# Performance work log

Hardware: AMD Instinct MI355X
Metric: run time of the kernel (lower is better)

## Reference

```python
import jax, jax.numpy as jnp
import numpy as np

GRID_SIZE = 5
SPLINE_ORDER = 3
GRID_LO, GRID_HI = -1.0, 1.0
N_COEFF = GRID_SIZE + SPLINE_ORDER  # 8


def make_grid(in_features):
    # (in_features, grid_size + 2*spline_order + 1) = (in, 12)
    h = (GRID_HI - GRID_LO) / GRID_SIZE
    g = jnp.arange(-SPLINE_ORDER, GRID_SIZE + SPLINE_ORDER + 1, dtype=jnp.float32) * h + GRID_LO
    return jnp.broadcast_to(g, (in_features, g.shape[0]))


def b_splines(x, grid):
    # x: (N, in); grid: (in, G). Returns (N, in, grid_size+spline_order).
    xe = x[..., None]
    bases = ((xe >= grid[:, :-1]) & (xe < grid[:, 1:])).astype(x.dtype)
    for k in range(1, SPLINE_ORDER + 1):
        left = (xe - grid[:, :-(k + 1)]) / (grid[:, k:-1] - grid[:, :-(k + 1)]) * bases[..., :-1]
        right = (grid[:, k + 1:] - xe) / (grid[:, k + 1:] - grid[:, 1:-k]) * bases[..., 1:]
        bases = left + right
    return bases


def kan_linear(x, base_w, spline_w, scaler, grid):
    # base branch: SiLU(x) @ base_w^T
    base_out = jax.nn.silu(x) @ base_w.T
    # spline branch: basis (N,in,c) contracted with scaled spline weight (out,in,c)
    b = b_splines(x, grid)
    sw = spline_w * scaler[..., None]
    spline_out = jnp.einsum('nic,oic->no', b, sw)
    return base_out + spline_out


def setup_inputs() -> dict:
    key = jax.random.key(0)
    ks = jax.random.split(key, 7)
    d_model, d_hid = 512, 2049  # d_ff + 1
    s = 0.1  # keep activations roughly inside grid range
    return {
        "x": jax.random.normal(ks[0], (4096, d_model), dtype=jnp.float32) * 0.3,
        "base_w1": jax.random.normal(ks[1], (d_hid, d_model), dtype=jnp.float32) * s,
        "spline_w1": jax.random.normal(ks[2], (d_hid, d_model, N_COEFF), dtype=jnp.float32) * s,
        "scaler1": jax.random.normal(ks[3], (d_hid, d_model), dtype=jnp.float32) * s,
        "base_w2": jax.random.normal(ks[4], (d_model, d_hid), dtype=jnp.float32) * s,
        "spline_w2": jax.random.normal(ks[5], (d_model, d_hid, N_COEFF), dtype=jnp.float32) * s,
        "scaler2": jax.random.normal(ks[6], (d_model, d_hid), dtype=jnp.float32) * s,
    }


def reference(x, base_w1, spline_w1, scaler1, base_w2, spline_w2, scaler2):
    grid1 = make_grid(x.shape[-1])
    h = kan_linear(x, base_w1, spline_w1, scaler1, grid1)
    grid2 = make_grid(h.shape[-1])
    out = kan_linear(h, base_w2, spline_w2, scaler2, grid2)
    return out
```

## Files before the change

kernel.cpp:

```cpp
#include <hip/hip_runtime.h>
#include <hip/hip_bf16.h>

#define T_TOK 4096
#define I1    512
#define O1    2049
#define O1P   2176
#define K1    4608
#define G1    64
#define I2    2049
#define O2    512
#define K2    18560
#define G2    271
#define SPLITS2 8
#define KLEN2 2368
#define NBY   32

typedef __attribute__((ext_vector_type(8))) short short8;
typedef __attribute__((ext_vector_type(4))) float floatx4;
typedef __attribute__((address_space(3))) void* lds_ptr_t;
typedef const __attribute__((address_space(1))) void* gmem_ptr_t;

__device__ __forceinline__ unsigned short f2bf(float f) {
  union { __hip_bfloat16 h; unsigned short u; } cv;
  cv.h = __float2bfloat16(f);
  return cv.u;
}
__device__ __forceinline__ unsigned bfr(float f) {
  union { float f; unsigned u; } c; c.f = f;
  return (c.u + 0x8000u) >> 16;
}
__device__ __forceinline__ float silu_f(float x) { return x / (1.0f + __expf(-x)); }

__device__ __forceinline__ uint4 spline_pack(float h) {
  float u = (h + 2.2f) * 2.5f;
  int ji = (int)u;
  ji = ji < 0 ? 0 : (ji > 10 ? 10 : ji);
  float t = u - (float)ji;
  float it = 1.0f - t, t2 = t * t, t3 = t2 * t;
  float b0 = it * it * it * (1.0f / 6.0f);
  float b1 = (3.0f * t3 - 6.0f * t2 + 4.0f) * (1.0f / 6.0f);
  float b2 = (-3.0f * t3 + 3.0f * t2 + 3.0f * t + 1.0f) * (1.0f / 6.0f);
  float b3 = t3 * (1.0f / 6.0f);
  unsigned pk01 = bfr(b0) | (bfr(b1) << 16);
  unsigned pk23 = bfr(b2) | (bfr(b3) << 16);
  unsigned long long p64 = (unsigned long long)pk01 | ((unsigned long long)pk23 << 32);
  bool inR = (h >= -2.2f) && (h < 2.2f);
  p64 = inR ? p64 : 0ull;
  int sh = (ji - 3) * 16;
  int shr = sh < 0 ? -sh : 0;
  int shl = sh < 0 ? 0 : sh;
  __uint128_t v = ((__uint128_t)(p64 >> shr)) << shl;
  union { __uint128_t q; uint4 u4; } cv;
  cv.q = v;
  return cv.u4;
}

__global__ void transpose_kernel(const float* __restrict__ src, float* __restrict__ dst,
                                 int R, int C) {
  __shared__ float t[32][33];
  int c0 = blockIdx.x * 32, r0 = blockIdx.y * 32;
  int tx = threadIdx.x & 31, ty = threadIdx.x >> 5;
#pragma unroll
  for (int i = 0; i < 32; i += 8)
    t[ty + i][tx] = src[(size_t)(r0 + ty + i) * C + c0 + tx];
  __syncthreads();
#pragma unroll
  for (int i = 0; i < 32; i += 8)
    dst[(size_t)(c0 + ty + i) * R + r0 + tx] = t[tx][ty + i];
}

__global__ void silu_pack_kernel(const float* __restrict__ St, uint4* __restrict__ SPK,
                                 int I, int M) {
  int m = blockIdx.x * 256 + threadIdx.x;
  int g = blockIdx.y;
  int off0 = g * 8;
  union { unsigned short s[8]; uint4 v; } pk;
#pragma unroll
  for (int c = 0; c < 8; ++c) {
    int off = off0 + c;
    float v = 0.0f;
    if (off < I) v = silu_f(St[(size_t)off * M + m]);
    pk.s[c] = f2bf(v);
  }
  SPK[(size_t)g * M + m] = pk.v;
}

__global__ void pack_w1_kernel(const float* __restrict__ bw, const float* __restrict__ sw,
                               const float* __restrict__ sc, unsigned short* __restrict__ W) {
  int k = blockIdx.x * 256 + threadIdx.x;
  int o = blockIdx.y;
  float v = 0.0f;
  if (o < O1) {
    if (k < 4096) v = sw[(size_t)o * 4096 + k] * sc[(size_t)o * I1 + (k >> 3)];
    else          v = bw[(size_t)o * I1 + (k - 4096)];
  }
  W[(size_t)o * K1 + k] = f2bf(v);
}

__global__ void pack_w2_kernel(const float* __restrict__ bw, const float* __restrict__ sw,
                               const float* __restrict__ sc, unsigned short* __restrict__ W) {
  int k = blockIdx.x * 256 + threadIdx.x;
  if (k >= K2) return;
  int o = blockIdx.y;
  float v = 0.0f;
  if (k < 16392)      v = sw[(size_t)o * 16392 + k] * sc[(size_t)o * I2 + (k >> 3)];
  else if (k < 18441) v = bw[(size_t)o * I2 + (k - 16392)];
  W[(size_t)o * K2 + k] = f2bf(v);
}

__global__ __launch_bounds__(256, 4)
void kan_gemm_kernel(const float* __restrict__ St, const uint4* __restrict__ SPK,
                     const unsigned short* __restrict__ Bw, float* __restrict__ C,
                     int I, int Ktot, int M, int N, int ldc, int kLen,
                     int nBx, int storeMode)
{
  __shared__ __align__(16) unsigned short As[128 * 64];
  __shared__ __align__(16) unsigned short Bs[128 * 64];

  const int Lb = blockIdx.x;
  const int m8 = Lb & 7;
  const int r  = Lb >> 3;
  const int bx = r % nBx;
  const int p  = m8 + ((r / nBx) << 3);
  const int by = p & (NBY - 1);
  const int bz = p >> 5;

  const int tid = threadIdx.x;
  const int ks = bz * kLen;
  int ke = ks + kLen; if (ke > Ktot) ke = Ktot;

  const int w = tid >> 6, L = tid & 63, q = L >> 4, ln = L & 15;
  const int wm = (w & 1) << 6, wn = (w >> 1) << 6;

  const int row = tid & 127;
  const int gh  = tid >> 7;
  const int mGlob = by * 128 + row;
  const float* s0  = St + mGlob;
  const uint4* sp0 = SPK + mGlob;

  floatx4 zf = {0.f, 0.f, 0.f, 0.f};
  floatx4 acc[4][4];
#pragma unroll
  for (int mt = 0; mt < 4; ++mt)
#pragma unroll
    for (int nt = 0; nt < 4; ++nt)
      acc[mt][nt] = zf;

  const unsigned short* gb[4];
  int ldsOff[4];
#pragma unroll
  for (int r4 = 0; r4 < 4; ++r4) {
    int e = r4 * 256 + tid;
    int br = e >> 3;
    int cg = (e & 7) ^ (br & 7);
    gb[r4] = Bw + ((long)bx * 128 + br) * (long)Ktot + ks + cg * 8;
    ldsOff[r4] = e * 8;
  }

  uint4 cur[4], nxt[4];
#pragma unroll
  for (int j2 = 0; j2 < 4; ++j2) {
    int gi = (ks >> 3) + gh * 4 + j2;
    if (gi < I) cur[j2].x = __float_as_uint(s0[(size_t)gi * M]);
    else        cur[j2]   = sp0[(size_t)(gi - I) * M];
  }

  for (int kc = ks; kc < ke; kc += 64) {
    __syncthreads();
#pragma unroll
    for (int r4 = 0; r4 < 4; ++r4) {
      __builtin_amdgcn_global_load_lds((gmem_ptr_t)gb[r4], (lds_ptr_t)&Bs[ldsOff[r4]], 16, 0, 0);
      gb[r4] += 64;
    }
    if (kc + 64 < ke) {
#pragma unroll
      for (int j2 = 0; j2 < 4; ++j2) {
        int gi = ((kc + 64) >> 3) + gh * 4 + j2;
        if (gi < I) nxt[j2].x = __float_as_uint(s0[(size_t)gi * M]);
        else        nxt[j2]   = sp0[(size_t)(gi - I) * M];
      }
    }

    const int gBase = (kc >> 3) + gh * 4;
#pragma unroll
    for (int j2 = 0; j2 < 4; ++j2) {
      int g  = gh * 4 + j2;
      int gi = gBase + j2;
      int pos = row * 64 + ((g ^ (row & 7)) << 3);
      uint4 val;
      if (gi < I) val = spline_pack(__uint_as_float(cur[j2].x));
      else        val = cur[j2];
      *(uint4*)&As[pos] = val;
    }
    __syncthreads();

#pragma unroll
    for (int s = 0; s < 2; ++s) {
      short8 af[4], bf[4];
#pragma unroll
      for (int mt = 0; mt < 4; ++mt) {
        int rr = wm + mt * 16 + ln;
        int cl = ((s << 2) | q) ^ (rr & 7);
        af[mt] = *(const short8*)&As[rr * 64 + cl * 8];
      }
#pragma unroll
      for (int nt = 0; nt < 4; ++nt) {
        int rr = wn + nt * 16 + ln;
        int cl = ((s << 2) | q) ^ (rr & 7);
        bf[nt] = *(const short8*)&Bs[rr * 64 + cl * 8];
      }
#pragma unroll
      for (int mt = 0; mt < 4; ++mt)
#pragma unroll
        for (int nt = 0; nt < 4; ++nt)
          acc[mt][nt] = __builtin_amdgcn_mfma_f32_16x16x32_bf16(af[mt], bf[nt], acc[mt][nt], 0, 0, 0);
    }
#pragma unroll
    for (int j2 = 0; j2 < 4; ++j2) cur[j2] = nxt[j2];
  }

  if (storeMode == 1) {
#pragma unroll
    for (int mt = 0; mt < 4; ++mt) {
#pragma unroll
      for (int nt = 0; nt < 4; ++nt) {
        int n = bx * 128 + wn + nt * 16 + ln;
        if (n < N) {
          int m0 = by * 128 + wm + mt * 16 + q * 4;
          *(float4*)&C[(size_t)n * ldc + m0] = *(float4*)&acc[mt][nt];
        }
      }
    }
  } else {
#pragma unroll
    for (int mt = 0; mt < 4; ++mt) {
#pragma unroll
      for (int nt = 0; nt < 4; ++nt) {
        int n = bx * 128 + wn + nt * 16 + ln;
        if (n < N) {
          int m0 = by * 128 + wm + mt * 16 + q * 4;
#pragma unroll
          for (int rg = 0; rg < 4; ++rg)
            atomicAdd(&C[(size_t)(m0 + rg) * ldc + n], acc[mt][nt][rg]);
        }
      }
    }
  }
}

extern "C" void kernel_launch(void* const* d_in, const int* in_sizes, int n_in,
                              void* d_out, int out_size, void* d_ws, size_t ws_size,
                              hipStream_t stream) {
  const float* x   = (const float*)d_in[0];
  const float* bw1 = (const float*)d_in[1];
  const float* sw1 = (const float*)d_in[2];
  const float* sc1 = (const float*)d_in[3];
  const float* bw2 = (const float*)d_in[4];
  const float* sw2 = (const float*)d_in[5];
  const float* sc2 = (const float*)d_in[6];
  float* out = (float*)d_out;

  float* Xt  = (float*)d_ws;
  float* H0t = Xt + (size_t)I1 * T_TOK;
  unsigned short* W1 = (unsigned short*)(H0t + (size_t)O1 * T_TOK);
  unsigned short* W2 = W1 + (size_t)O1P * K1;
  uint4* SPK1 = (uint4*)(W2 + (size_t)O2 * K2);
  uint4* SPK2 = SPK1 + (size_t)G1 * T_TOK;

  hipMemsetAsync(d_out, 0, (size_t)out_size * sizeof(float), stream);

  transpose_kernel<<<dim3(I1 / 32, T_TOK / 32), 256, 0, stream>>>(x, Xt, T_TOK, I1);
  pack_w1_kernel<<<dim3(K1 / 256, O1P), 256, 0, stream>>>(bw1, sw1, sc1, W1);
  pack_w2_kernel<<<dim3((K2 + 255) / 256, O2), 256, 0, stream>>>(bw2, sw2, sc2, W2);
  silu_pack_kernel<<<dim3(T_TOK / 256, G1), 256, 0, stream>>>(Xt, SPK1, I1, T_TOK);

  kan_gemm_kernel<<<O1P / 128 * NBY, 256, 0, stream>>>(
      Xt, SPK1, W1, H0t, I1, K1, T_TOK, O1, T_TOK, K1, O1P / 128, 1);

  silu_pack_kernel<<<dim3(T_TOK / 256, G2), 256, 0, stream>>>(H0t, SPK2, I2, T_TOK);

  kan_gemm_kernel<<<O2 / 128 * NBY * SPLITS2, 256, 0, stream>>>(
      H0t, SPK2, W2, out, I2, K2, T_TOK, O2, O2, KLEN2, O2 / 128, 2);
}
```

Before: 505.5 us.

## Pre-materialize layer-1 bf16 activations, DMA both GEMM operands, widen layer-2 tiles

Layer 1 now precomputes the full spline-basis and SiLU bf16 activation matrix in row-major form, so the GEMM can load both operands straight into LDS with global_load_lds instead of evaluating splines inside the main loop. Layer 1 also gains a 2-way K split with atomic accumulation, which needs an extra memset of the hidden buffer. Layer 2 moves to a 512-thread kernel with 128x256 tiles and 12 K splits, which improves B reuse and adds parallelism. The costs are extra HBM traffic for the materialized A1 and more atomics.

```diff
diff --git a/kernel.cpp b/kernel.cpp
--- a/kernel.cpp
+++ b/kernel.cpp
@@ -6,14 +6,15 @@
 #define O1    2049
 #define O1P   2176
 #define K1    4608
-#define G1    64
+#define NG1   576
+#define SPLITS1 2
+#define KLEN1 2304
 #define I2    2049
 #define O2    512
 #define K2    18560
 #define G2    271
-#define SPLITS2 8
-#define KLEN2 2368
-#define NBY   32
+#define SPLITS2 12
+#define KLEN2 1600
 
 typedef __attribute__((ext_vector_type(8))) short short8;
 typedef __attribute__((ext_vector_type(4))) float floatx4;
@@ -55,18 +56,27 @@
   return cv.u4;
 }
 
-__global__ void transpose_kernel(const float* __restrict__ src, float* __restrict__ dst,
-                                 int R, int C) {
-  __shared__ float t[32][33];
-  int c0 = blockIdx.x * 32, r0 = blockIdx.y * 32;
-  int tx = threadIdx.x & 31, ty = threadIdx.x >> 5;
-#pragma unroll
-  for (int i = 0; i < 32; i += 8)
-    t[ty + i][tx] = src[(size_t)(r0 + ty + i) * C + c0 + tx];
-  __syncthreads();
-#pragma unroll
-  for (int i = 0; i < 32; i += 8)
-    dst[(size_t)(c0 + ty + i) * R + r0 + tx] = t[tx][ty + i];
+__global__ void pack_a1_kernel(const float* __restrict__ x, uint4* __restrict__ A1u) {
+  int wv = threadIdx.x >> 6;
+  int lane = threadIdx.x & 63;
+  int m = blockIdx.x * 4 + wv;
+  const float* xr = x + (size_t)m * I1;
+  uint4* arow = A1u + (size_t)m * NG1;
+#pragma unroll
+  for (int i = 0; i < 8; ++i) {
+    int g = i * 64 + lane;
+    arow[g] = spline_pack(xr[g]);
+  }
+  {
+    union { unsigned short s[8]; uint4 v; } pk;
+    const float4* xq = (const float4*)(xr + lane * 8);
+    float4 f0 = xq[0], f1 = xq[1];
+    pk.s[0] = f2bf(silu_f(f0.x)); pk.s[1] = f2bf(silu_f(f0.y));
+    pk.s[2] = f2bf(silu_f(f0.z)); pk.s[3] = f2bf(silu_f(f0.w));
+    pk.s[4] = f2bf(silu_f(f1.x)); pk.s[5] = f2bf(silu_f(f1.y));
+    pk.s[6] = f2bf(silu_f(f1.z)); pk.s[7] = f2bf(silu_f(f1.w));
+    arow[512 + lane] = pk.v;
+  }
 }
 
 __global__ void silu_pack_kernel(const float* __restrict__ St, uint4* __restrict__ SPK,
@@ -109,91 +119,49 @@
 }
 
 __global__ __launch_bounds__(256, 4)
-void kan_gemm_kernel(const float* __restrict__ St, const uint4* __restrict__ SPK,
-                     const unsigned short* __restrict__ Bw, float* __restrict__ C,
-                     int I, int Ktot, int M, int N, int ldc, int kLen,
-                     int nBx, int storeMode)
+void gemm_dma_kernel(const unsigned short* __restrict__ A,
+                     const unsigned short* __restrict__ Bw,
+                     float* __restrict__ C)
 {
   __shared__ __align__(16) unsigned short As[128 * 64];
   __shared__ __align__(16) unsigned short Bs[128 * 64];
 
   const int Lb = blockIdx.x;
-  const int m8 = Lb & 7;
-  const int r  = Lb >> 3;
-  const int bx = r % nBx;
-  const int p  = m8 + ((r / nBx) << 3);
-  const int by = p & (NBY - 1);
-  const int bz = p >> 5;
+  const int m8 = Lb & 7, r = Lb >> 3;
+  const int bx = r % 17;
+  const int t  = r / 17;
+  const int by = m8 + ((t & 3) << 3);
+  const int bz = t >> 2;
+  const int ks = bz * KLEN1;
 
   const int tid = threadIdx.x;
-  const int ks = bz * kLen;
-  int ke = ks + kLen; if (ke > Ktot) ke = Ktot;
-
   const int w = tid >> 6, L = tid & 63, q = L >> 4, ln = L & 15;
   const int wm = (w & 1) << 6, wn = (w >> 1) << 6;
 
-  const int row = tid & 127;
-  const int gh  = tid >> 7;
-  const int mGlob = by * 128 + row;
-  const float* s0  = St + mGlob;
-  const uint4* sp0 = SPK + mGlob;
-
   floatx4 zf = {0.f, 0.f, 0.f, 0.f};
   floatx4 acc[4][4];
 #pragma unroll
   for (int mt = 0; mt < 4; ++mt)
 #pragma unroll
-    for (int nt = 0; nt < 4; ++nt)
-      acc[mt][nt] = zf;
-
-  const unsigned short* gb[4];
-  int ldsOff[4];
-#pragma unroll
-  for (int r4 = 0; r4 < 4; ++r4) {
-    int e = r4 * 256 + tid;
-    int br = e >> 3;
-    int cg = (e & 7) ^ (br & 7);
-    gb[r4] = Bw + ((long)bx * 128 + br) * (long)Ktot + ks + cg * 8;
-    ldsOff[r4] = e * 8;
-  }
-
-  uint4 cur[4], nxt[4];
-#pragma unroll
-  for (int j2 = 0; j2 < 4; ++j2) {
-    int gi = (ks >> 3) + gh * 4 + j2;
-    if (gi < I) cur[j2].x = __float_as_uint(s0[(size_t)gi * M]);
-    else        cur[j2]   = sp0[(size_t)(gi - I) * M];
-  }
-
-  for (int kc = ks; kc < ke; kc += 64) {
+    for (int nt = 0; nt < 4; ++nt) acc[mt][nt] = zf;
+
+  const int rowS = tid >> 3;
+  const int cg = (tid & 7) ^ (rowS & 7);
+  const unsigned short* ga = A  + ((long)by * 128 + rowS) * K1 + ks + cg * 8;
+  const unsigned short* gb = Bw + ((long)bx * 128 + rowS) * K1 + ks + cg * 8;
+  const int ldsT = tid * 8;
+
+  for (int it = 0; it < KLEN1 / 64; ++it) {
     __syncthreads();
 #pragma unroll
     for (int r4 = 0; r4 < 4; ++r4) {
-      __builtin_amdgcn_global_load_lds((gmem_ptr_t)gb[r4], (lds_ptr_t)&Bs[ldsOff[r4]], 16, 0, 0);
-      gb[r4] += 64;
-    }
-    if (kc + 64 < ke) {
-#pragma unroll
-      for (int j2 = 0; j2 < 4; ++j2) {
-        int gi = ((kc + 64) >> 3) + gh * 4 + j2;
-        if (gi < I) nxt[j2].x = __float_as_uint(s0[(size_t)gi * M]);
-        else        nxt[j2]   = sp0[(size_t)(gi - I) * M];
-      }
-    }
-
-    const int gBase = (kc >> 3) + gh * 4;
-#pragma unroll
-    for (int j2 = 0; j2 < 4; ++j2) {
-      int g  = gh * 4 + j2;
-      int gi = gBase + j2;
-      int pos = row * 64 + ((g ^ (row & 7)) << 3);
-      uint4 val;
-      if (gi < I) val = spline_pack(__uint_as_float(cur[j2].x));
-      else        val = cur[j2];
-      *(uint4*)&As[pos] = val;
-    }
+      __builtin_amdgcn_global_load_lds((gmem_ptr_t)(ga + (long)r4 * 32 * K1),
+                                       (lds_ptr_t)&As[r4 * 2048 + ldsT], 16, 0, 0);
+      __builtin_amdgcn_global_load_lds((gmem_ptr_t)(gb + (long)r4 * 32 * K1),
+                                       (lds_ptr_t)&Bs[r4 * 2048 + ldsT], 16, 0, 0);
+    }
+    ga += 64; gb += 64;
     __syncthreads();
-
 #pragma unroll
     for (int s = 0; s < 2; ++s) {
       short8 af[4], bf[4];
@@ -215,35 +183,130 @@
         for (int nt = 0; nt < 4; ++nt)
           acc[mt][nt] = __builtin_amdgcn_mfma_f32_16x16x32_bf16(af[mt], bf[nt], acc[mt][nt], 0, 0, 0);
     }
-#pragma unroll
-    for (int j2 = 0; j2 < 4; ++j2) cur[j2] = nxt[j2];
-  }
-
-  if (storeMode == 1) {
-#pragma unroll
-    for (int mt = 0; mt < 4; ++mt) {
+  }
+
+#pragma unroll
+  for (int mt = 0; mt < 4; ++mt) {
+#pragma unroll
+    for (int nt = 0; nt < 4; ++nt) {
+      int n = bx * 128 + wn + nt * 16 + ln;
+      if (n < O1) {
+        int m0 = by * 128 + wm + mt * 16 + q * 4;
+        float* cp = &C[(size_t)n * T_TOK + m0];
+#pragma unroll
+        for (int rg = 0; rg < 4; ++rg) atomicAdd(cp + rg, acc[mt][nt][rg]);
+      }
+    }
+  }
+}
+
+__global__ __launch_bounds__(512, 4)
+void kan_gemm256_kernel(const float* __restrict__ St, const uint4* __restrict__ SPK,
+                        const unsigned short* __restrict__ Bw, float* __restrict__ C)
+{
+  __shared__ __align__(16) unsigned short As[128 * 64];
+  __shared__ __align__(16) unsigned short Bs[256 * 64];
+
+  const int Lb = blockIdx.x;
+  const int m8 = Lb & 7, r = Lb >> 3;
+  const int bx = r & 1;
+  const int t  = r >> 1;
+  const int by = m8 + ((t & 3) << 3);
+  const int bz = t >> 2;
+  const int ks = bz * KLEN2;
+  int ke = ks + KLEN2; if (ke > K2) ke = K2;
+
+  const int tid = threadIdx.x;
+  const int w = tid >> 6, L = tid & 63, q = L >> 4, ln = L & 15;
+  const int wm = (w & 1) << 6, wn = (w >> 1) << 6;
+
+  const int row = tid & 127;
+  const int gh  = tid >> 7;
+  const float* s0  = St  + by * 128 + row;
+  const uint4* sp0 = SPK + by * 128 + row;
+
+  floatx4 zf = {0.f, 0.f, 0.f, 0.f};
+  floatx4 acc[4][4];
+#pragma unroll
+  for (int mt = 0; mt < 4; ++mt)
+#pragma unroll
+    for (int nt = 0; nt < 4; ++nt) acc[mt][nt] = zf;
+
+  const int rowB = tid >> 3;
+  const int cgB = (tid & 7) ^ (rowB & 7);
+  const unsigned short* gb = Bw + ((long)bx * 256 + rowB) * K2 + ks + cgB * 8;
+  const int ldsT = tid * 8;
+
+  uint4 cur[2], nxt[2];
+#pragma unroll
+  for (int j2 = 0; j2 < 2; ++j2) {
+    int gi = (ks >> 3) + gh * 2 + j2;
+    if (gi < I2) cur[j2].x = __float_as_uint(s0[(size_t)gi * T_TOK]);
+    else         cur[j2]   = sp0[(size_t)(gi - I2) * T_TOK];
+  }
+
+  for (int kc = ks; kc < ke; kc += 64) {
+    __syncthreads();
+#pragma unroll
+    for (int r4 = 0; r4 < 4; ++r4)
+      __builtin_amdgcn_global_load_lds((gmem_ptr_t)(gb + (long)r4 * 64 * K2),
+                                       (lds_ptr_t)&Bs[r4 * 4096 + ldsT], 16, 0, 0);
+    gb += 64;
+
+    if (kc + 64 < ke) {
+#pragma unroll
+      for (int j2 = 0; j2 < 2; ++j2) {
+        int gi = ((kc + 64) >> 3) + gh * 2 + j2;
+        if (gi < I2) nxt[j2].x = __float_as_uint(s0[(size_t)gi * T_TOK]);
+        else         nxt[j2]   = sp0[(size_t)(gi - I2) * T_TOK];
+      }
+    }
+
+    const int gBase = kc >> 3;
+#pragma unroll
+    for (int j2 = 0; j2 < 2; ++j2) {
+      int g  = gh * 2 + j2;
+      int gi = gBase + g;
+      int pos = row * 64 + ((g ^ (row & 7)) << 3);
+      uint4 val = (gi < I2) ? spline_pack(__uint_as_float(cur[j2].x)) : cur[j2];
+      *(uint4*)&As[pos] = val;
+    }
+    __syncthreads();
+
+#pragma unroll
+    for (int s = 0; s < 2; ++s) {
+      short8 af[4], bf[4];
+#pragma unroll
+      for (int mt = 0; mt < 4; ++mt) {
+        int rr = wm + mt * 16 + ln;
+        int cl = ((s << 2) | q) ^ (rr & 7);
+        af[mt] = *(const short8*)&As[rr * 64 + cl * 8];
+      }
 #pragma unroll
       for (int nt = 0; nt < 4; ++nt) {
-        int n = bx * 128 + wn + nt * 16 + ln;
-        if (n < N) {
-          int m0 = by * 128 + wm + mt * 16 + q * 4;
-          *(float4*)&C[(size_t)n * ldc + m0] = *(float4*)&acc[mt][nt];
-        }
-      }
-    }
-  } else {
-#pragma unroll
-    for (int mt = 0; mt < 4; ++mt) {
-#pragma unroll
-      for (int nt = 0; nt < 4; ++nt) {
-        int n = bx * 128 + wn + nt * 16 + ln;
-        if (n < N) {
-          int m0 = by * 128 + wm + mt * 16 + q * 4;
-#pragma unroll
-          for (int rg = 0; rg < 4; ++rg)
-            atomicAdd(&C[(size_t)(m0 + rg) * ldc + n], acc[mt][nt][rg]);
-        }
-      }
+        int rr = wn + nt * 16 + ln;
+        int cl = ((s << 2) | q) ^ (rr & 7);
+        bf[nt] = *(const short8*)&Bs[rr * 64 + cl * 8];
+      }
+#pragma unroll
+      for (int mt = 0; mt < 4; ++mt)
+#pragma unroll
+        for (int nt = 0; nt < 4; ++nt)
+          acc[mt][nt] = __builtin_amdgcn_mfma_f32_16x16x32_bf16(af[mt], bf[nt], acc[mt][nt], 0, 0, 0);
+    }
+#pragma unroll
+    for (int j2 = 0; j2 < 2; ++j2) cur[j2] = nxt[j2];
+  }
+
+#pragma unroll
+  for (int mt = 0; mt < 4; ++mt) {
+#pragma unroll
+    for (int nt = 0; nt < 4; ++nt) {
+      int n = bx * 256 + wn + nt * 16 + ln;
+      int m0 = by * 128 + wm + mt * 16 + q * 4;
+#pragma unroll
+      for (int rg = 0; rg < 4; ++rg)
+        atomicAdd(&C[(size_t)(m0 + rg) * O2 + n], acc[mt][nt][rg]);
     }
   }
 }
@@ -260,25 +323,23 @@
   const float* sc2 = (const float*)d_in[6];
   float* out = (float*)d_out;
 
-  float* Xt  = (float*)d_ws;
-  float* H0t = Xt + (size_t)I1 * T_TOK;
+  uint4* A1u = (uint4*)d_ws;
+  float* H0t = (float*)(A1u + (size_t)T_TOK * NG1);
   unsigned short* W1 = (unsigned short*)(H0t + (size_t)O1 * T_TOK);
   unsigned short* W2 = W1 + (size_t)O1P * K1;
-  uint4* SPK1 = (uint4*)(W2 + (size_t)O2 * K2);
-  uint4* SPK2 = SPK1 + (size_t)G1 * T_TOK;
+  uint4* SPK2 = (uint4*)(W2 + (size_t)O2 * K2);
 
   hipMemsetAsync(d_out, 0, (size_t)out_size * sizeof(float), stream);
-
-  transpose_kernel<<<dim3(I1 / 32, T_TOK / 32), 256, 0, stream>>>(x, Xt, T_TOK, I1);
+  hipMemsetAsync(H0t, 0, (size_t)O1 * T_TOK * sizeof(float), stream);
+
+  pack_a1_kernel<<<T_TOK / 4, 256, 0, stream>>>(x, A1u);
   pack_w1_kernel<<<dim3(K1 / 256, O1P), 256, 0, stream>>>(bw1, sw1, sc1, W1);
   pack_w2_kernel<<<dim3((K2 + 255) / 256, O2), 256, 0, stream>>>(bw2, sw2, sc2, W2);
-  silu_pack_kernel<<<dim3(T_TOK / 256, G1), 256, 0, stream>>>(Xt, SPK1, I1, T_TOK);
-
-  kan_gemm_kernel<<<O1P / 128 * NBY, 256, 0, stream>>>(
-      Xt, SPK1, W1, H0t, I1, K1, T_TOK, O1, T_TOK, K1, O1P / 128, 1);
+
+  gemm_dma_kernel<<<8 * 17 * 4 * SPLITS1, 256, 0, stream>>>(
+      (const unsigned short*)A1u, W1, H0t);
 
   silu_pack_kernel<<<dim3(T_TOK / 256, G2), 256, 0, stream>>>(H0t, SPK2, I2, T_TOK);
 
-  kan_gemm_kernel<<<O2 / 128 * NBY * SPLITS2, 256, 0, stream>>>(
-      H0t, SPK2, W2, out, I2, K2, T_TOK, O2, O2, KLEN2, O2 / 128, 2);
-}
+  kan_gemm256_kernel<<<8 * 2 * 4 * SPLITS2, 512, 0, stream>>>(H0t, SPK2, W2, out);
+}
```

Result: slower. 614.8 us (+21.6%).

## Double-buffer LDS tiles in KAN GEMM to overlap loads with MFMA

Applied to the files above, without the earlier changes.

Splits the A and B shared-memory tiles into two buffers so that the next K-chunk's async B loads and the spline-packed A writes go into the alternate buffer while MFMAs run on the current one. This removes one barrier per iteration. LDS use doubles to 64KB per block, so launch bounds drop from 4 to 2 blocks per SM, trading occupancy for overlap. The block-index mapping is rewritten inline and the NBY macro is dropped; grid sizes are unchanged.

```diff
diff --git a/kernel.cpp b/kernel.cpp
--- a/kernel.cpp
+++ b/kernel.cpp
@@ -13,7 +13,6 @@
 #define G2    271
 #define SPLITS2 8
 #define KLEN2 2368
-#define NBY   32
 
 typedef __attribute__((ext_vector_type(8))) short short8;
 typedef __attribute__((ext_vector_type(4))) float floatx4;
@@ -108,91 +107,106 @@
   W[(size_t)o * K2 + k] = f2bf(v);
 }
 
-__global__ __launch_bounds__(256, 4)
-void kan_gemm_kernel(const float* __restrict__ St, const uint4* __restrict__ SPK,
-                     const unsigned short* __restrict__ Bw, float* __restrict__ C,
-                     int I, int Ktot, int M, int N, int ldc, int kLen,
-                     int nBx, int storeMode)
+__global__ __launch_bounds__(256, 2)
+void kan_gemm_db_kernel(const float* __restrict__ St, const uint4* __restrict__ SPK,
+                        const unsigned short* __restrict__ Bw, float* __restrict__ C,
+                        int I, int Ktot, int M, int N, int ldc, int kLen,
+                        int nBx, int storeMode)
 {
-  __shared__ __align__(16) unsigned short As[128 * 64];
-  __shared__ __align__(16) unsigned short Bs[128 * 64];
+  __shared__ __align__(16) unsigned short As[2][128 * 64];
+  __shared__ __align__(16) unsigned short Bs[2][128 * 64];
 
   const int Lb = blockIdx.x;
-  const int m8 = Lb & 7;
-  const int r  = Lb >> 3;
+  const int m8 = Lb & 7, r = Lb >> 3;
   const int bx = r % nBx;
-  const int p  = m8 + ((r / nBx) << 3);
-  const int by = p & (NBY - 1);
-  const int bz = p >> 5;
-
-  const int tid = threadIdx.x;
+  const int t  = r / nBx;
+  const int by = m8 + ((t & 3) << 3);
+  const int bz = t >> 2;
   const int ks = bz * kLen;
   int ke = ks + kLen; if (ke > Ktot) ke = Ktot;
-
+  const int nIter = (ke - ks) >> 6;
+
+  const int tid = threadIdx.x;
   const int w = tid >> 6, L = tid & 63, q = L >> 4, ln = L & 15;
   const int wm = (w & 1) << 6, wn = (w >> 1) << 6;
 
   const int row = tid & 127;
   const int gh  = tid >> 7;
-  const int mGlob = by * 128 + row;
-  const float* s0  = St + mGlob;
-  const uint4* sp0 = SPK + mGlob;
+  const float* s0  = St  + by * 128 + row;
+  const uint4* sp0 = SPK + by * 128 + row;
 
   floatx4 zf = {0.f, 0.f, 0.f, 0.f};
   floatx4 acc[4][4];
 #pragma unroll
   for (int mt = 0; mt < 4; ++mt)
 #pragma unroll
-    for (int nt = 0; nt < 4; ++nt)
-      acc[mt][nt] = zf;
-
-  const unsigned short* gb[4];
-  int ldsOff[4];
-#pragma unroll
-  for (int r4 = 0; r4 < 4; ++r4) {
-    int e = r4 * 256 + tid;
-    int br = e >> 3;
-    int cg = (e & 7) ^ (br & 7);
-    gb[r4] = Bw + ((long)bx * 128 + br) * (long)Ktot + ks + cg * 8;
-    ldsOff[r4] = e * 8;
-  }
-
-  uint4 cur[4], nxt[4];
-#pragma unroll
-  for (int j2 = 0; j2 < 4; ++j2) {
-    int gi = (ks >> 3) + gh * 4 + j2;
-    if (gi < I) cur[j2].x = __float_as_uint(s0[(size_t)gi * M]);
-    else        cur[j2]   = sp0[(size_t)(gi - I) * M];
-  }
-
-  for (int kc = ks; kc < ke; kc += 64) {
+    for (int nt = 0; nt < 4; ++nt) acc[mt][nt] = zf;
+
+  const int rowB = tid >> 3;
+  const int cgB = (tid & 7) ^ (rowB & 7);
+  const unsigned short* gb0 = Bw + ((long)bx * 128 + rowB) * (long)Ktot + ks + cgB * 8;
+  const int ldsT = tid * 8;
+
+  uint4 cur[4];
+  {
+    int gBase = (ks >> 3) + gh * 4;
+#pragma unroll
+    for (int j = 0; j < 4; ++j) {
+      int gi = gBase + j;
+      if (gi < I) cur[j].x = __float_as_uint(s0[(size_t)gi * M]);
+      else        cur[j]   = sp0[(size_t)(gi - I) * M];
+    }
+#pragma unroll
+    for (int r4 = 0; r4 < 4; ++r4)
+      __builtin_amdgcn_global_load_lds((gmem_ptr_t)(gb0 + (long)r4 * 32 * Ktot),
+                                       (lds_ptr_t)&Bs[0][r4 * 2048 + ldsT], 16, 0, 0);
+#pragma unroll
+    for (int j = 0; j < 4; ++j) {
+      int g = gh * 4 + j;
+      int gi = gBase + j;
+      int pos = row * 64 + ((g ^ (row & 7)) << 3);
+      uint4 val = (gi < I) ? spline_pack(__uint_as_float(cur[j].x)) : cur[j];
+      *(uint4*)&As[0][pos] = val;
+    }
+    if (nIter > 1) {
+      int gB1 = ((ks + 64) >> 3) + gh * 4;
+#pragma unroll
+      for (int j = 0; j < 4; ++j) {
+        int gi = gB1 + j;
+        if (gi < I) cur[j].x = __float_as_uint(s0[(size_t)gi * M]);
+        else        cur[j]   = sp0[(size_t)(gi - I) * M];
+      }
+    }
+  }
+
+  for (int i = 0; i < nIter; ++i) {
+    const int c = i & 1;
     __syncthreads();
-#pragma unroll
-    for (int r4 = 0; r4 < 4; ++r4) {
-      __builtin_amdgcn_global_load_lds((gmem_ptr_t)gb[r4], (lds_ptr_t)&Bs[ldsOff[r4]], 16, 0, 0);
-      gb[r4] += 64;
-    }
-    if (kc + 64 < ke) {
-#pragma unroll
-      for (int j2 = 0; j2 < 4; ++j2) {
-        int gi = ((kc + 64) >> 3) + gh * 4 + j2;
-        if (gi < I) nxt[j2].x = __float_as_uint(s0[(size_t)gi * M]);
-        else        nxt[j2]   = sp0[(size_t)(gi - I) * M];
-      }
-    }
-
-    const int gBase = (kc >> 3) + gh * 4;
-#pragma unroll
-    for (int j2 = 0; j2 < 4; ++j2) {
-      int g  = gh * 4 + j2;
-      int gi = gBase + j2;
-      int pos = row * 64 + ((g ^ (row & 7)) << 3);
-      uint4 val;
-      if (gi < I) val = spline_pack(__uint_as_float(cur[j2].x));
-      else        val = cur[j2];
-      *(uint4*)&As[pos] = val;
-    }
-    __syncthreads();
+    if (i + 1 < nIter) {
+      const unsigned short* g = gb0 + (long)(i + 1) * 64;
+#pragma unroll
+      for (int r4 = 0; r4 < 4; ++r4)
+        __builtin_amdgcn_global_load_lds((gmem_ptr_t)(g + (long)r4 * 32 * Ktot),
+                                         (lds_ptr_t)&Bs[1 - c][r4 * 2048 + ldsT], 16, 0, 0);
+      int gBase = ((ks + (i + 1) * 64) >> 3) + gh * 4;
+#pragma unroll
+      for (int j = 0; j < 4; ++j) {
+        int g2 = gh * 4 + j;
+        int gi = gBase + j;
+        int pos = row * 64 + ((g2 ^ (row & 7)) << 3);
+        uint4 val = (gi < I) ? spline_pack(__uint_as_float(cur[j].x)) : cur[j];
+        *(uint4*)&As[1 - c][pos] = val;
+      }
+      if (i + 2 < nIter) {
+        int gB2 = ((ks + (i + 2) * 64) >> 3) + gh * 4;
+#pragma unroll
+        for (int j = 0; j < 4; ++j) {
+          int gi = gB2 + j;
+          if (gi < I) cur[j].x = __float_as_uint(s0[(size_t)gi * M]);
+          else        cur[j]   = sp0[(size_t)(gi - I) * M];
+        }
+      }
+    }
 
 #pragma unroll
     for (int s = 0; s < 2; ++s) {
@@ -201,13 +215,13 @@
       for (int mt = 0; mt < 4; ++mt) {
         int rr = wm + mt * 16 + ln;
         int cl = ((s << 2) | q) ^ (rr & 7);
-        af[mt] = *(const short8*)&As[rr * 64 + cl * 8];
+        af[mt] = *(const short8*)&As[c][rr * 64 + cl * 8];
       }
 #pragma unroll
       for (int nt = 0; nt < 4; ++nt) {
         int rr = wn + nt * 16 + ln;
         int cl = ((s << 2) | q) ^ (rr & 7);
-        bf[nt] = *(const short8*)&Bs[rr * 64 + cl * 8];
+        bf[nt] = *(const short8*)&Bs[c][rr * 64 + cl * 8];
       }
 #pragma unroll
       for (int mt = 0; mt < 4; ++mt)
@@ -215,8 +229,6 @@
         for (int nt = 0; nt < 4; ++nt)
           acc[mt][nt] = __builtin_amdgcn_mfma_f32_16x16x32_bf16(af[mt], bf[nt], acc[mt][nt], 0, 0, 0);
     }
-#pragma unroll
-    for (int j2 = 0; j2 < 4; ++j2) cur[j2] = nxt[j2];
   }
 
   if (storeMode == 1) {
@@ -274,11 +286,11 @@
   pack_w2_kernel<<<dim3((K2 + 255) / 256, O2), 256, 0, stream>>>(bw2, sw2, sc2, W2);
   silu_pack_kernel<<<dim3(T_TOK / 256, G1), 256, 0, stream>>>(Xt, SPK1, I1, T_TOK);
 
-  kan_gemm_kernel<<<O1P / 128 * NBY, 256, 0, stream>>>(
-      Xt, SPK1, W1, H0t, I1, K1, T_TOK, O1, T_TOK, K1, O1P / 128, 1);
+  kan_gemm_db_kernel<<<8 * 17 * 4, 256, 0, stream>>>(
+      Xt, SPK1, W1, H0t, I1, K1, T_TOK, O1, T_TOK, K1, 17, 1);
 
   silu_pack_kernel<<<dim3(T_TOK / 256, G2), 256, 0, stream>>>(H0t, SPK2, I2, T_TOK);
 
-  kan_gemm_kernel<<<O2 / 128 * NBY * SPLITS2, 256, 0, stream>>>(
-      H0t, SPK2, W2, out, I2, K2, T_TOK, O2, O2, KLEN2, O2 / 128, 2);
-}
+  kan_gemm_db_kernel<<<8 * 4 * 4 * SPLITS2, 256, 0, stream>>>(
+      H0t, SPK2, W2, out, I2, K2, T_TOK, O2, O2, KLEN2, 4, 2);
+}
```

After: 575.2 us. 1.14x slower.
